# Kernel optimization log

Hardware: AMD Instinct MI355X
Metric: run time of the kernel (lower is better)

Reference implementation:

```python
import jax, jax.numpy as jnp
import numpy as np

TOKENS, DIM, DIM_OUT, R, ALPHA = 8192, 4096, 4096, 16, 32
SCALE = ALPHA / R  # 2.0


def setup_inputs() -> dict:
    key = jax.random.key(0)
    k1, k2, k3, k4, k5 = jax.random.split(key, 5)
    x = jax.random.normal(k1, (TOKENS, DIM), dtype=jnp.float32)
    A = jax.random.normal(k2, (DIM, R), dtype=jnp.float32)
    B = jax.random.normal(k3, (R, DIM_OUT), dtype=jnp.float32) * 0.02
    W = jax.random.normal(k4, (DIM_OUT, DIM), dtype=jnp.float32) * 0.02  # base Linear weight
    b = jax.random.normal(k5, (DIM_OUT,), dtype=jnp.float32)
    return {"x": x, "A": A, "B": B, "W": W, "b": b}


def reference(x, A, B, W, b):
    # LoRA path: x @ (A @ B) * scale, computed in the efficient low-rank order
    # (mathematically identical to materializing the full-rank weight).
    lora = ((x @ A) @ B) * SCALE              # [tokens, dim_out]
    base = x @ W.T + b                         # wrapped base Linear forward
    return lora + base
```

## Files before the change

kernel.cpp:

```cpp
#include <hip/hip_runtime.h>
#include <hip/hip_bf16.h>
#include <stdint.h>

#define TOKENS   8192
#define DIM      4096
#define DIM_OUT  4096
#define LORA_R   16
#define LORA_SCALE 2.0f

typedef __bf16 bf16_t;
typedef __attribute__((ext_vector_type(8))) __bf16 bfrag;
typedef __attribute__((ext_vector_type(4))) float f32x4;

__device__ __forceinline__ void gload_lds16(const bf16_t* gsrc, bf16_t* ldst) {
    __builtin_amdgcn_global_load_lds(
        (const __attribute__((address_space(1))) uint32_t*)(const void*)gsrc,
        (__attribute__((address_space(3))) uint32_t*)(void*)ldst,
        16, 0, 0);
}

#define CAST_BLOCKS 2048
__global__ void prep_kernel(const float* __restrict__ x, bf16_t* __restrict__ xb,
                            const float* __restrict__ W, const float* __restrict__ A,
                            const float* __restrict__ B, bf16_t* __restrict__ Wt) {
    if (blockIdx.x < CAST_BLOCKS) {
        const int total = TOKENS * DIM / 8;
        for (int i = blockIdx.x * blockDim.x + threadIdx.x; i < total;
             i += CAST_BLOCKS * 256) {
            const float4* p = reinterpret_cast<const float4*>(x + (size_t)i * 8);
            float4 v0 = p[0], v1 = p[1];
            union { bf16_t o[8]; uint4 u; } pk;
            pk.o[0] = (bf16_t)v0.x; pk.o[1] = (bf16_t)v0.y;
            pk.o[2] = (bf16_t)v0.z; pk.o[3] = (bf16_t)v0.w;
            pk.o[4] = (bf16_t)v1.x; pk.o[5] = (bf16_t)v1.y;
            pk.o[6] = (bf16_t)v1.z; pk.o[7] = (bf16_t)v1.w;
            *reinterpret_cast<uint4*>(xb + (size_t)i * 8) = pk.u;
        }
    } else {
        int idx = (blockIdx.x - CAST_BLOCKS) * blockDim.x + threadIdx.x;
        int k0 = (idx & 511) << 3;
        int n0 = (idx >> 9) << 2;

        float bn[4][16];
#pragma unroll
        for (int r = 0; r < 16; ++r) {
            float4 bv = *reinterpret_cast<const float4*>(B + (size_t)r * DIM_OUT + n0);
            bn[0][r] = bv.x; bn[1][r] = bv.y; bn[2][r] = bv.z; bn[3][r] = bv.w;
        }
        float ab[4][8];
#pragma unroll
        for (int j = 0; j < 8; ++j) {
            const float4* ap = reinterpret_cast<const float4*>(A + (size_t)(k0 + j) * LORA_R);
            float4 a0 = ap[0], a1 = ap[1], a2 = ap[2], a3 = ap[3];
            float av[16] = {a0.x,a0.y,a0.z,a0.w,a1.x,a1.y,a1.z,a1.w,
                            a2.x,a2.y,a2.z,a2.w,a3.x,a3.y,a3.z,a3.w};
#pragma unroll
            for (int n = 0; n < 4; ++n) {
                float s = 0.f;
#pragma unroll
                for (int r = 0; r < 16; ++r) s += av[r] * bn[n][r];
                ab[n][j] = s;
            }
        }
#pragma unroll
        for (int n = 0; n < 4; ++n) {
            const float4* wp = reinterpret_cast<const float4*>(W + (size_t)(n0 + n) * DIM + k0);
            float4 w0 = wp[0], w1 = wp[1];
            float wv[8] = {w0.x,w0.y,w0.z,w0.w,w1.x,w1.y,w1.z,w1.w};
            union { bf16_t o[8]; uint4 u; } pk;
#pragma unroll
            for (int j = 0; j < 8; ++j) pk.o[j] = (bf16_t)(wv[j] + LORA_SCALE * ab[n][j]);
            *reinterpret_cast<uint4*>(Wt + (size_t)(n0 + n) * DIM + k0) = pk.u;
        }
    }
}

#define BM 256
#define BN 256
#define BK 64
#define MB_BLKS (TOKENS / BM)
#define NB_BLKS (DIM_OUT / BN)
#define NT      (DIM / BK)

#define SB0() __builtin_amdgcn_sched_barrier(0)
#define VMWAIT_(n) asm volatile("s_waitcnt vmcnt(" #n ")" ::: "memory")
#define VMWAIT(n) VMWAIT_(n)

__global__ __launch_bounds__(512, 2) void gemm_kernel(
    const bf16_t* __restrict__ Xb, const bf16_t* __restrict__ Wt,
    const float* __restrict__ bias, float* __restrict__ C)
{
    __shared__ __align__(16) bf16_t sA[2][BM][BK];
    __shared__ __align__(16) bf16_t sB[2][BN][BK];

    int bid = blockIdx.x;
    int xcd = bid & 7;
    int j   = bid >> 3;
    int qq  = j >> 5;
    int rr  = j & 31;
    int bm  = xcd * 4 + (rr >> 3);
    int bn  = (rr & 7) + 8 * qq;

    const int tid  = threadIdx.x;
    const int lane = tid & 63;
    const int wid  = tid >> 6;
    const int wr   = wid >> 2;
    const int wc   = wid & 3;

    const int srow = tid >> 3;
    const int scol = (tid & 7) * 8;
    const int koff = (((tid & 7) ^ ((tid >> 3) & 7)) * 8);
    const bf16_t* Ag = Xb + (size_t)(bm * BM + srow) * DIM + koff;
    const bf16_t* Bg = Wt + (size_t)(bn * BN + srow) * DIM + koff;

#define STAGE_A_H(dd, kt, h) do { \
    const bf16_t* s_ = Ag + (size_t)(kt) * BK + (size_t)((h) * 128) * DIM; \
    bf16_t* d_ = &sA[dd][(h) * 128 + srow][scol]; \
    gload_lds16(s_,                    d_); \
    gload_lds16(s_ + (size_t)64 * DIM, d_ + 64 * BK); \
} while (0)

#define STAGE_B_H(dd, kt, h) do { \
    const bf16_t* s_ = Bg + (size_t)(kt) * BK + (size_t)((h) * 128) * DIM; \
    bf16_t* d_ = &sB[dd][(h) * 128 + srow][scol]; \
    gload_lds16(s_,                    d_); \
    gload_lds16(s_ + (size_t)64 * DIM, d_ + 64 * BK); \
} while (0)

    const int q     = lane & 7;
    const int kslot = lane >> 4;
    const int r15   = lane & 15;
    const int cK0   = ((kslot    ) ^ q) * 8;
    const int cK1   = ((kslot + 4) ^ q) * 8;
    const int arow0 = wr * 128 + r15;
    const int brow0 = wc * 64  + r15;

    f32x4 acc[8][4] = {};
    bfrag a[4][2], bLo[2][2], bHi[2][2];

#define READ_A4(dd, mb) do { \
    _Pragma("unroll") \
    for (int m_ = 0; m_ < 4; ++m_) { \
        a[m_][0] = *reinterpret_cast<const bfrag*>(&sA[dd][arow0 + (mb + m_) * 16][cK0]); \
        a[m_][1] = *reinterpret_cast<const bfrag*>(&sA[dd][arow0 + (mb + m_) * 16][cK1]); \
    } \
} while (0)

#define READ_B2(dst, dd, nb) do { \
    _Pragma("unroll") \
    for (int n_ = 0; n_ < 2; ++n_) { \
        dst[n_][0] = *reinterpret_cast<const bfrag*>(&sB[dd][brow0 + (nb + n_) * 16][cK0]); \
        dst[n_][1] = *reinterpret_cast<const bfrag*>(&sB[dd][brow0 + (nb + n_) * 16][cK1]); \
    } \
} while (0)

#define PSYNC() do { \
    __builtin_amdgcn_s_barrier(); \
    asm volatile("s_waitcnt lgkmcnt(0)" ::: "memory"); \
    SB0(); \
} while (0)

#define MFMA_Q(Bf, mb, nb) do { \
    __builtin_amdgcn_s_setprio(1); \
    _Pragma("unroll") \
    for (int m_ = 0; m_ < 4; ++m_) \
    _Pragma("unroll") \
    for (int n_ = 0; n_ < 2; ++n_) \
    _Pragma("unroll") \
    for (int ks_ = 0; ks_ < 2; ++ks_) \
        acc[mb + m_][nb + n_] = __builtin_amdgcn_mfma_f32_16x16x32_bf16( \
            a[m_][ks_], Bf[n_][ks_], acc[mb + m_][nb + n_], 0, 0, 0); \
    __builtin_amdgcn_s_setprio(0); \
} while (0)

#define EBAR() __builtin_amdgcn_s_barrier()

#define TILEPAIR(u, S, VMn) do { \
     READ_A4(0, 0); READ_B2(bLo, 0, 0); STAGE_A_H(1, (u) + 1, 0); \
             PSYNC(); MFMA_Q(bLo, 0, 0); EBAR(); \
     READ_B2(bHi, 0, 2); STAGE_A_H(1, (u) + 1, 1); \
             PSYNC(); MFMA_Q(bHi, 0, 2); EBAR(); \
     READ_A4(0, 4); if (S) STAGE_B_H(0, (u) + 2, 0); \
             PSYNC(); MFMA_Q(bHi, 4, 2); EBAR(); \
     if (S) STAGE_B_H(0, (u) + 2, 1); \
             __builtin_amdgcn_s_barrier(); \
             MFMA_Q(bLo, 4, 0); VMWAIT(VMn); EBAR(); \
     READ_A4(1, 0); READ_B2(bLo, 1, 0); if (S) STAGE_A_H(0, (u) + 2, 0); \
             PSYNC(); MFMA_Q(bLo, 0, 0); EBAR(); \
     READ_B2(bHi, 1, 2); if (S) STAGE_A_H(0, (u) + 2, 1); \
             PSYNC(); MFMA_Q(bHi, 0, 2); EBAR(); \
     READ_A4(1, 4); if (S) STAGE_B_H(1, (u) + 3, 0); \
             PSYNC(); MFMA_Q(bHi, 4, 2); EBAR(); \
     if (S) STAGE_B_H(1, (u) + 3, 1); \
             __builtin_amdgcn_s_barrier(); \
             MFMA_Q(bLo, 4, 0); VMWAIT(0); EBAR(); \
} while (0)

    STAGE_A_H(0, 0, 0); STAGE_A_H(0, 0, 1);
    STAGE_B_H(0, 0, 0); STAGE_B_H(0, 0, 1);
    STAGE_B_H(1, 1, 0); STAGE_B_H(1, 1, 1);
    VMWAIT(4);
    EBAR();

    for (int it = 0; it < NT / 2 - 1; ++it) {
        int u = 2 * it;
         READ_A4(0, 0); READ_B2(bLo, 0, 0); STAGE_A_H(1, u + 1, 0);
                 PSYNC(); MFMA_Q(bLo, 0, 0); EBAR();
         READ_B2(bHi, 0, 2); STAGE_A_H(1, u + 1, 1);
                 PSYNC(); MFMA_Q(bHi, 0, 2); EBAR();
         READ_A4(0, 4); STAGE_B_H(0, u + 2, 0);
                 PSYNC(); MFMA_Q(bHi, 4, 2); EBAR();
         STAGE_B_H(0, u + 2, 1);
                 __builtin_amdgcn_s_barrier();
                 MFMA_Q(bLo, 4, 0); VMWAIT(4); EBAR();
         READ_A4(1, 0); READ_B2(bLo, 1, 0); STAGE_A_H(0, u + 2, 0);
                 PSYNC(); MFMA_Q(bLo, 0, 0); EBAR();
         READ_B2(bHi, 1, 2); STAGE_A_H(0, u + 2, 1);
                 PSYNC(); MFMA_Q(bHi, 0, 2); EBAR();
         READ_A4(1, 4); STAGE_B_H(1, u + 3, 0);
                 PSYNC(); MFMA_Q(bHi, 4, 2); EBAR();
         STAGE_B_H(1, u + 3, 1);
                 __builtin_amdgcn_s_barrier();
                 MFMA_Q(bLo, 4, 0); VMWAIT(4); EBAR();
    }
     READ_A4(0, 0); READ_B2(bLo, 0, 0); STAGE_A_H(1, 63, 0);
             PSYNC(); MFMA_Q(bLo, 0, 0); EBAR();
     READ_B2(bHi, 0, 2); STAGE_A_H(1, 63, 1);
             PSYNC(); MFMA_Q(bHi, 0, 2); EBAR();
     READ_A4(0, 4);
             PSYNC(); MFMA_Q(bHi, 4, 2); EBAR();
     __builtin_amdgcn_s_barrier();
             MFMA_Q(bLo, 4, 0); VMWAIT(0); EBAR();
     READ_A4(1, 0); READ_B2(bLo, 1, 0);
             PSYNC(); MFMA_Q(bLo, 0, 0); EBAR();
     READ_B2(bHi, 1, 2);
             PSYNC(); MFMA_Q(bHi, 0, 2); EBAR();
     READ_A4(1, 4);
             PSYNC(); MFMA_Q(bHi, 4, 2); EBAR();
     MFMA_Q(bLo, 4, 0);

    int row0 = bm * BM + wr * 128 + (lane >> 4) * 4;
    int col0 = bn * BN + wc * 64 + r15;
#pragma unroll
    for (int n = 0; n < 4; ++n) {
        int c = col0 + n * 16;
        float bv = bias[c];
#pragma unroll
        for (int m = 0; m < 8; ++m) {
            int r = row0 + m * 16;
#pragma unroll
            for (int jj = 0; jj < 4; ++jj)
                C[(size_t)(r + jj) * DIM_OUT + c] = acc[m][n][jj] + bv;
        }
    }
}

extern "C" void kernel_launch(void* const* d_in, const int* in_sizes, int n_in,
                              void* d_out, int out_size, void* d_ws, size_t ws_size,
                              hipStream_t stream) {
    const float* x = (const float*)d_in[0];
    const float* A = (const float*)d_in[1];
    const float* B = (const float*)d_in[2];
    const float* W = (const float*)d_in[3];
    const float* b = (const float*)d_in[4];
    float* out = (float*)d_out;

    bf16_t* xb = (bf16_t*)d_ws;
    bf16_t* Wt = (bf16_t*)((char*)d_ws + (size_t)TOKENS * DIM * 2);

    prep_kernel<<<CAST_BLOCKS + 2048, 256, 0, stream>>>(x, xb, W, A, B, Wt);
    gemm_kernel<<<MB_BLKS * NB_BLKS, 512, 0, stream>>>(xb, Wt, b, out);
}
```

Measured before the change: 327.5 us.

## Fuse fp32-to-bf16 cast of x into GEMM A-tile loading

Removes the separate pass that converts x to bf16 in workspace. The GEMM now loads fp32 x tiles into registers, converts them to bf16 and writes them to LDS inside the pipelined main loop, while W tiles still use direct global-to-LDS loads. This saves one 128MB read plus 64MB write round trip, but the GEMM now reads twice the bytes for A, each x row is re-read by all 16 column blocks, and register pressure and VALU work rise inside the MFMA loop.

```diff
diff --git a/kernel.cpp b/kernel.cpp
--- a/kernel.cpp
+++ b/kernel.cpp
@@ -19,59 +19,42 @@
         16, 0, 0);
 }
 
-#define CAST_BLOCKS 2048
-__global__ void prep_kernel(const float* __restrict__ x, bf16_t* __restrict__ xb,
-                            const float* __restrict__ W, const float* __restrict__ A,
+__global__ void weff_kernel(const float* __restrict__ W, const float* __restrict__ A,
                             const float* __restrict__ B, bf16_t* __restrict__ Wt) {
-    if (blockIdx.x < CAST_BLOCKS) {
-        const int total = TOKENS * DIM / 8;
-        for (int i = blockIdx.x * blockDim.x + threadIdx.x; i < total;
-             i += CAST_BLOCKS * 256) {
-            const float4* p = reinterpret_cast<const float4*>(x + (size_t)i * 8);
-            float4 v0 = p[0], v1 = p[1];
-            union { bf16_t o[8]; uint4 u; } pk;
-            pk.o[0] = (bf16_t)v0.x; pk.o[1] = (bf16_t)v0.y;
-            pk.o[2] = (bf16_t)v0.z; pk.o[3] = (bf16_t)v0.w;
-            pk.o[4] = (bf16_t)v1.x; pk.o[5] = (bf16_t)v1.y;
-            pk.o[6] = (bf16_t)v1.z; pk.o[7] = (bf16_t)v1.w;
-            *reinterpret_cast<uint4*>(xb + (size_t)i * 8) = pk.u;
+    int idx = blockIdx.x * blockDim.x + threadIdx.x;
+    int k0 = (idx & 511) << 3;
+    int n0 = (idx >> 9) << 2;
+
+    float bn[4][16];
+#pragma unroll
+    for (int r = 0; r < 16; ++r) {
+        float4 bv = *reinterpret_cast<const float4*>(B + (size_t)r * DIM_OUT + n0);
+        bn[0][r] = bv.x; bn[1][r] = bv.y; bn[2][r] = bv.z; bn[3][r] = bv.w;
+    }
+    float ab[4][8];
+#pragma unroll
+    for (int j = 0; j < 8; ++j) {
+        const float4* ap = reinterpret_cast<const float4*>(A + (size_t)(k0 + j) * LORA_R);
+        float4 a0 = ap[0], a1 = ap[1], a2 = ap[2], a3 = ap[3];
+        float av[16] = {a0.x,a0.y,a0.z,a0.w,a1.x,a1.y,a1.z,a1.w,
+                        a2.x,a2.y,a2.z,a2.w,a3.x,a3.y,a3.z,a3.w};
+#pragma unroll
+        for (int n = 0; n < 4; ++n) {
+            float s = 0.f;
+#pragma unroll
+            for (int r = 0; r < 16; ++r) s += av[r] * bn[n][r];
+            ab[n][j] = s;
         }
-    } else {
-        int idx = (blockIdx.x - CAST_BLOCKS) * blockDim.x + threadIdx.x;
-        int k0 = (idx & 511) << 3;
-        int n0 = (idx >> 9) << 2;
-
-        float bn[4][16];
-#pragma unroll
-        for (int r = 0; r < 16; ++r) {
-            float4 bv = *reinterpret_cast<const float4*>(B + (size_t)r * DIM_OUT + n0);
-            bn[0][r] = bv.x; bn[1][r] = bv.y; bn[2][r] = bv.z; bn[3][r] = bv.w;
-        }
-        float ab[4][8];
-#pragma unroll
-        for (int j = 0; j < 8; ++j) {
-            const float4* ap = reinterpret_cast<const float4*>(A + (size_t)(k0 + j) * LORA_R);
-            float4 a0 = ap[0], a1 = ap[1], a2 = ap[2], a3 = ap[3];
-            float av[16] = {a0.x,a0.y,a0.z,a0.w,a1.x,a1.y,a1.z,a1.w,
-                            a2.x,a2.y,a2.z,a2.w,a3.x,a3.y,a3.z,a3.w};
-#pragma unroll
-            for (int n = 0; n < 4; ++n) {
-                float s = 0.f;
-#pragma unroll
-                for (int r = 0; r < 16; ++r) s += av[r] * bn[n][r];
-                ab[n][j] = s;
-            }
-        }
-#pragma unroll
-        for (int n = 0; n < 4; ++n) {
-            const float4* wp = reinterpret_cast<const float4*>(W + (size_t)(n0 + n) * DIM + k0);
-            float4 w0 = wp[0], w1 = wp[1];
-            float wv[8] = {w0.x,w0.y,w0.z,w0.w,w1.x,w1.y,w1.z,w1.w};
-            union { bf16_t o[8]; uint4 u; } pk;
-#pragma unroll
-            for (int j = 0; j < 8; ++j) pk.o[j] = (bf16_t)(wv[j] + LORA_SCALE * ab[n][j]);
-            *reinterpret_cast<uint4*>(Wt + (size_t)(n0 + n) * DIM + k0) = pk.u;
-        }
+    }
+#pragma unroll
+    for (int n = 0; n < 4; ++n) {
+        const float4* wp = reinterpret_cast<const float4*>(W + (size_t)(n0 + n) * DIM + k0);
+        float4 w0 = wp[0], w1 = wp[1];
+        float wv[8] = {w0.x,w0.y,w0.z,w0.w,w1.x,w1.y,w1.z,w1.w};
+        union { bf16_t o[8]; uint4 u; } pk;
+#pragma unroll
+        for (int j = 0; j < 8; ++j) pk.o[j] = (bf16_t)(wv[j] + LORA_SCALE * ab[n][j]);
+        *reinterpret_cast<uint4*>(Wt + (size_t)(n0 + n) * DIM + k0) = pk.u;
     }
 }
 
@@ -87,7 +70,7 @@
 #define VMWAIT(n) VMWAIT_(n)
 
 __global__ __launch_bounds__(512, 2) void gemm_kernel(
-    const bf16_t* __restrict__ Xb, const bf16_t* __restrict__ Wt,
+    const float* __restrict__ X, const bf16_t* __restrict__ Wt,
     const float* __restrict__ bias, float* __restrict__ C)
 {
     __shared__ __align__(16) bf16_t sA[2][BM][BK];
@@ -110,14 +93,42 @@
     const int srow = tid >> 3;
     const int scol = (tid & 7) * 8;
     const int koff = (((tid & 7) ^ ((tid >> 3) & 7)) * 8);
-    const bf16_t* Ag = Xb + (size_t)(bm * BM + srow) * DIM + koff;
+    const float*  Xg = X  + (size_t)(bm * BM + srow) * DIM + koff;
     const bf16_t* Bg = Wt + (size_t)(bn * BN + srow) * DIM + koff;
 
-#define STAGE_A_H(dd, kt, h) do { \
-    const bf16_t* s_ = Ag + (size_t)(kt) * BK + (size_t)((h) * 128) * DIM; \
-    bf16_t* d_ = &sA[dd][(h) * 128 + srow][scol]; \
-    gload_lds16(s_,                    d_); \
-    gload_lds16(s_ + (size_t)64 * DIM, d_ + 64 * BK); \
+    float4 xa0, xa1, xa2, xa3, xb0, xb1, xb2, xb3;
+#define LOADX2(kt) do { \
+    const float* s0_ = Xg + (size_t)(kt) * BK; \
+    const float* s1_ = s0_ + (size_t)128 * DIM; \
+    xa0 = *reinterpret_cast<const float4*>(s0_); \
+    xa1 = *reinterpret_cast<const float4*>(s0_ + 4); \
+    xa2 = *reinterpret_cast<const float4*>(s0_ + (size_t)64 * DIM); \
+    xa3 = *reinterpret_cast<const float4*>(s0_ + (size_t)64 * DIM + 4); \
+    xb0 = *reinterpret_cast<const float4*>(s1_); \
+    xb1 = *reinterpret_cast<const float4*>(s1_ + 4); \
+    xb2 = *reinterpret_cast<const float4*>(s1_ + (size_t)64 * DIM); \
+    xb3 = *reinterpret_cast<const float4*>(s1_ + (size_t)64 * DIM + 4); \
+} while (0)
+
+#define CVT8(u_, f0, f1) do { \
+    u_.o[0] = (bf16_t)f0.x; u_.o[1] = (bf16_t)f0.y; \
+    u_.o[2] = (bf16_t)f0.z; u_.o[3] = (bf16_t)f0.w; \
+    u_.o[4] = (bf16_t)f1.x; u_.o[5] = (bf16_t)f1.y; \
+    u_.o[6] = (bf16_t)f1.z; u_.o[7] = (bf16_t)f1.w; \
+} while (0)
+
+#define WRITEX_A(dd) do { \
+    union { bf16_t o[8]; uint4 u; } p0_, p1_; \
+    CVT8(p0_, xa0, xa1); CVT8(p1_, xa2, xa3); \
+    *reinterpret_cast<uint4*>(&sA[dd][srow][scol]) = p0_.u; \
+    *reinterpret_cast<uint4*>(&sA[dd][64 + srow][scol]) = p1_.u; \
+} while (0)
+
+#define WRITEX_B(dd) do { \
+    union { bf16_t o[8]; uint4 u; } p0_, p1_; \
+    CVT8(p0_, xb0, xb1); CVT8(p1_, xb2, xb3); \
+    *reinterpret_cast<uint4*>(&sA[dd][128 + srow][scol]) = p0_.u; \
+    *reinterpret_cast<uint4*>(&sA[dd][192 + srow][scol]) = p1_.u; \
 } while (0)
 
 #define STAGE_B_H(dd, kt, h) do { \
@@ -175,59 +186,41 @@
 
 #define EBAR() __builtin_amdgcn_s_barrier()
 
-#define TILEPAIR(u, S, VMn) do { \
-     READ_A4(0, 0); READ_B2(bLo, 0, 0); STAGE_A_H(1, (u) + 1, 0); \
-             PSYNC(); MFMA_Q(bLo, 0, 0); EBAR(); \
-     READ_B2(bHi, 0, 2); STAGE_A_H(1, (u) + 1, 1); \
-             PSYNC(); MFMA_Q(bHi, 0, 2); EBAR(); \
-     READ_A4(0, 4); if (S) STAGE_B_H(0, (u) + 2, 0); \
-             PSYNC(); MFMA_Q(bHi, 4, 2); EBAR(); \
-     if (S) STAGE_B_H(0, (u) + 2, 1); \
-             __builtin_amdgcn_s_barrier(); \
-             MFMA_Q(bLo, 4, 0); VMWAIT(VMn); EBAR(); \
-     READ_A4(1, 0); READ_B2(bLo, 1, 0); if (S) STAGE_A_H(0, (u) + 2, 0); \
-             PSYNC(); MFMA_Q(bLo, 0, 0); EBAR(); \
-     READ_B2(bHi, 1, 2); if (S) STAGE_A_H(0, (u) + 2, 1); \
-             PSYNC(); MFMA_Q(bHi, 0, 2); EBAR(); \
-     READ_A4(1, 4); if (S) STAGE_B_H(1, (u) + 3, 0); \
-             PSYNC(); MFMA_Q(bHi, 4, 2); EBAR(); \
-     if (S) STAGE_B_H(1, (u) + 3, 1); \
-             __builtin_amdgcn_s_barrier(); \
-             MFMA_Q(bLo, 4, 0); VMWAIT(0); EBAR(); \
-} while (0)
-
-    STAGE_A_H(0, 0, 0); STAGE_A_H(0, 0, 1);
+    LOADX2(0);
+    WRITEX_A(0);
+    WRITEX_B(0);
     STAGE_B_H(0, 0, 0); STAGE_B_H(0, 0, 1);
     STAGE_B_H(1, 1, 0); STAGE_B_H(1, 1, 1);
     VMWAIT(4);
+    asm volatile("s_waitcnt lgkmcnt(0)" ::: "memory");
     EBAR();
 
     for (int it = 0; it < NT / 2 - 1; ++it) {
         int u = 2 * it;
-         READ_A4(0, 0); READ_B2(bLo, 0, 0); STAGE_A_H(1, u + 1, 0);
+         READ_A4(0, 0); READ_B2(bLo, 0, 0); LOADX2(u + 1);
                  PSYNC(); MFMA_Q(bLo, 0, 0); EBAR();
-         READ_B2(bHi, 0, 2); STAGE_A_H(1, u + 1, 1);
+         READ_B2(bHi, 0, 2); WRITEX_A(1);
                  PSYNC(); MFMA_Q(bHi, 0, 2); EBAR();
-         READ_A4(0, 4); STAGE_B_H(0, u + 2, 0);
+         READ_A4(0, 4); WRITEX_B(1); STAGE_B_H(0, u + 2, 0);
                  PSYNC(); MFMA_Q(bHi, 4, 2); EBAR();
          STAGE_B_H(0, u + 2, 1);
                  __builtin_amdgcn_s_barrier();
                  MFMA_Q(bLo, 4, 0); VMWAIT(4); EBAR();
-         READ_A4(1, 0); READ_B2(bLo, 1, 0); STAGE_A_H(0, u + 2, 0);
+         READ_A4(1, 0); READ_B2(bLo, 1, 0); LOADX2(u + 2);
                  PSYNC(); MFMA_Q(bLo, 0, 0); EBAR();
-         READ_B2(bHi, 1, 2); STAGE_A_H(0, u + 2, 1);
+         READ_B2(bHi, 1, 2); WRITEX_A(0);
                  PSYNC(); MFMA_Q(bHi, 0, 2); EBAR();
-         READ_A4(1, 4); STAGE_B_H(1, u + 3, 0);
+         READ_A4(1, 4); WRITEX_B(0); STAGE_B_H(1, u + 3, 0);
                  PSYNC(); MFMA_Q(bHi, 4, 2); EBAR();
          STAGE_B_H(1, u + 3, 1);
                  __builtin_amdgcn_s_barrier();
                  MFMA_Q(bLo, 4, 0); VMWAIT(4); EBAR();
     }
-     READ_A4(0, 0); READ_B2(bLo, 0, 0); STAGE_A_H(1, 63, 0);
+     READ_A4(0, 0); READ_B2(bLo, 0, 0); LOADX2(63);
              PSYNC(); MFMA_Q(bLo, 0, 0); EBAR();
-     READ_B2(bHi, 0, 2); STAGE_A_H(1, 63, 1);
+     READ_B2(bHi, 0, 2); WRITEX_A(1);
              PSYNC(); MFMA_Q(bHi, 0, 2); EBAR();
-     READ_A4(0, 4);
+     READ_A4(0, 4); WRITEX_B(1);
              PSYNC(); MFMA_Q(bHi, 4, 2); EBAR();
      __builtin_amdgcn_s_barrier();
              MFMA_Q(bLo, 4, 0); VMWAIT(0); EBAR();
@@ -265,9 +258,8 @@
     const float* b = (const float*)d_in[4];
     float* out = (float*)d_out;
 
-    bf16_t* xb = (bf16_t*)d_ws;
-    bf16_t* Wt = (bf16_t*)((char*)d_ws + (size_t)TOKENS * DIM * 2);
-
-    prep_kernel<<<CAST_BLOCKS + 2048, 256, 0, stream>>>(x, xb, W, A, B, Wt);
-    gemm_kernel<<<MB_BLKS * NB_BLKS, 512, 0, stream>>>(xb, Wt, b, out);
-}
+    bf16_t* Wt = (bf16_t*)d_ws;
+
+    weff_kernel<<<(DIM_OUT * DIM / 32) / 256, 256, 0, stream>>>(W, A, B, Wt);
+    gemm_kernel<<<MB_BLKS * NB_BLKS, 512, 0, stream>>>(x, Wt, b, out);
+}
```

Result: slower. 409.5 us (+25.0%).
